# Kernel optimization log

Measured on AMD Instinct MI355X. Metric: run time of the kernel, lower is better.

## Reference

```python
import jax, jax.numpy as jnp
import numpy as np

N = 8192
C_IN = 512
C_INTER = 128  # in_channels // unit_nums = 512 // 4


def setup_inputs() -> dict:
    key = jax.random.key(0)
    ks = jax.random.split(key, 6)
    x = jax.random.normal(ks[0], (N, C_IN), dtype=jnp.float32)
    # Linear weights init: normal(0, 0.01); biases zero. Stored as [in, out].
    Wg = 0.01 * jax.random.normal(ks[1], (C_IN, C_INTER), dtype=jnp.float32)
    Wt = 0.01 * jax.random.normal(ks[2], (C_IN, C_INTER), dtype=jnp.float32)
    Wp = 0.01 * jax.random.normal(ks[3], (C_IN, C_INTER), dtype=jnp.float32)
    bg = jnp.zeros((C_INTER,), dtype=jnp.float32)
    bt = jnp.zeros((C_INTER,), dtype=jnp.float32)
    bp = jnp.zeros((C_INTER,), dtype=jnp.float32)
    # 1x1 conv weight (1, 2*C_INTER, 1, 1) flattened: first half hits theta, second half phi
    wcat = 0.01 * jax.random.normal(ks[4], (2 * C_INTER,), dtype=jnp.float32)
    return {"x": x, "Wg": Wg, "bg": bg, "Wt": Wt, "bt": bt, "Wp": Wp, "bp": bp, "wcat": wcat}


def reference(x, Wg, bg, Wt, bt, Wp, bp, wcat):
    n = x.shape[0]
    g_x = x @ Wg + bg          # [N, C_inter]
    theta = x @ Wt + bt        # [N, C_inter]
    phi = x @ Wp + bp          # [N, C_inter]
    c = theta.shape[1]
    # 1x1 conv over cat([theta_i, phi_j]) == w1.theta_i + w2.phi_j (outer sum), then ReLU
    a = theta @ wcat[:c]       # [N]
    b = phi @ wcat[c:]         # [N]
    f = jax.nn.relu(a[:, None] + b[None, :])  # [N, N]
    z = (f / n) @ g_x          # [N, C_inter]
    return z
```

## Files before the change

### kernel.cpp

```cpp
#include <hip/hip_runtime.h>

#define C_IN   512
#define C_INT  128
#define NBUCK  8192
#define SEG    32
#define NSEG   256

typedef short short8 __attribute__((ext_vector_type(8)));
typedef float floatx4 __attribute__((ext_vector_type(4)));


__device__ __forceinline__ int bucket_of(float v, float bmin, float inv_w) {
    float fk = (v - bmin) * inv_w;
    fk = fminf(fmaxf(fk, 0.f), (float)(NBUCK - 1));
    return (int)fk;
}

__device__ __forceinline__ short bf16rnd(float v) {
    unsigned u = __float_as_uint(v);
    return (short)((u + 0x7fffu + ((u >> 16) & 1u)) >> 16);
}


__global__ __launch_bounds__(256) void prep_kernel(
        const float* __restrict__ Wt, const float* __restrict__ Wp,
        const float* __restrict__ Wg, const float* __restrict__ wcat,
        const float* __restrict__ bt, const float* __restrict__ bp,
        float* __restrict__ ut, float* __restrict__ up, float* __restrict__ scal,
        unsigned short* __restrict__ WgT) {
    int t = threadIdx.x, bk = blockIdx.x;
    if (bk < 16) {
        const float* W  = (bk < 8) ? Wt : Wp;
        const float* wv = wcat + ((bk < 8) ? 0 : C_INT);
        float* dst      = (bk < 8) ? ut : up;
        int k = (bk & 7) * 64 + (t >> 2);
        int q = t & 3;
        const float4* row = (const float4*)(W + (size_t)k * C_INT);
        const float4* cv4 = (const float4*)wv;
        float s = 0.f;
        #pragma unroll
        for (int i = 0; i < 8; ++i) {
            float4 a = row[q * 8 + i];
            float4 c = cv4[q * 8 + i];
            s += a.x * c.x + a.y * c.y + a.z * c.z + a.w * c.w;
        }
        s += __shfl_xor(s, 1);
        s += __shfl_xor(s, 2);
        if (q == 0) dst[k] = s;
    } else if (bk == 16) {
        float sumsq = 0.f;
        const float4* w2v = (const float4*)(wcat + C_INT);
        for (int r = 0; r < 2; ++r) {
            int k = t * 2 + r;
            const float4* row = (const float4*)(Wp + (size_t)k * C_INT);
            float d = 0.f;
            #pragma unroll
            for (int i = 0; i < 32; ++i) {
                float4 a4 = row[i]; float4 c4 = w2v[i];
                d += a4.x * c4.x + a4.y * c4.y + a4.z * c4.z + a4.w * c4.w;
            }
            sumsq += d * d;
        }
        float s1p = (t < C_INT) ? bt[t] * wcat[t] : 0.f;
        float s2p = (t < C_INT) ? bp[t] * wcat[C_INT + t] : 0.f;
        for (int off = 32; off; off >>= 1) {
            s1p   += __shfl_down(s1p, off);
            s2p   += __shfl_down(s2p, off);
            sumsq += __shfl_down(sumsq, off);
        }
        __shared__ float red[12];
        int w = t >> 6, lane = t & 63;
        if (lane == 0) { red[w] = s1p; red[4 + w] = s2p; red[8 + w] = sumsq; }
        __syncthreads();
        if (t == 0) {
            float s0 = red[0] + red[1] + red[2] + red[3];
            float s1 = red[4] + red[5] + red[6] + red[7];
            float sq = red[8] + red[9] + red[10] + red[11];
            float sigma = sqrtf(sq);
            scal[0] = s0; scal[1] = s1;
            if (sigma > 1e-20f) {
                scal[2] = s1 - 8.f * sigma;
                scal[3] = (float)NBUCK / (16.f * sigma);
            } else {
                scal[2] = s1 - 1.f; scal[3] = 0.f;
            }
        }
    } else {
        __shared__ float tile[64][132];
        int kb = (bk - 17) * 64;
        #pragma unroll
        for (int it = 0; it < 8; ++it) {
            int idx = it * 256 + t;
            int r = idx >> 5, c4 = idx & 31;
            *(float4*)&tile[r][c4 * 4] =
                ((const float4*)(Wg + (size_t)(kb + r) * C_INT))[c4];
        }
        __syncthreads();
        int n = t & 127, kc = (t >> 7) * 32;
        unsigned pk[16];
        #pragma unroll
        for (int i = 0; i < 16; ++i) {
            unsigned lo = (unsigned short)bf16rnd(tile[kc + 2 * i][n]);
            unsigned hi = (unsigned short)bf16rnd(tile[kc + 2 * i + 1][n]);
            pk[i] = lo | (hi << 16);
        }
        uint4* dst = (uint4*)(WgT + (size_t)n * C_IN + kb + kc);
        #pragma unroll
        for (int i2 = 0; i2 < 4; ++i2) dst[i2] = *(uint4*)&pk[i2 * 4];
    }
}


__global__ __launch_bounds__(64) void gemm_mfma(
        const float* __restrict__ x, const unsigned short* __restrict__ WgT,
        const float* __restrict__ bg,
        const float* __restrict__ ut, const float* __restrict__ up,
        const float* __restrict__ scal,
        _Float16* __restrict__ g, float* __restrict__ a, float* __restrict__ b) {
    int lane = threadIdx.x;
    int i0 = blockIdx.x * 16;
    int m = lane & 15, q = lane >> 4;
    floatx4 accg[8] = {};
    floatx4 accab = {};
    const float* xrow = x + (size_t)(i0 + m) * C_IN + q * 8;
    const float* absrc = (m == 0) ? ut : up;
    #pragma unroll
    for (int ks = 0; ks < 16; ++ks) {
        int k0 = ks * 32;
        float4 f0 = *(const float4*)(xrow + k0);
        float4 f1 = *(const float4*)(xrow + k0 + 4);
        short8 af;
        af[0] = bf16rnd(f0.x); af[1] = bf16rnd(f0.y);
        af[2] = bf16rnd(f0.z); af[3] = bf16rnd(f0.w);
        af[4] = bf16rnd(f1.x); af[5] = bf16rnd(f1.y);
        af[6] = bf16rnd(f1.z); af[7] = bf16rnd(f1.w);
        short8 abf = {};
        if (m < 2) {
            float4 u0 = *(const float4*)(absrc + k0 + q * 8);
            float4 u1 = *(const float4*)(absrc + k0 + q * 8 + 4);
            abf[0] = bf16rnd(u0.x); abf[1] = bf16rnd(u0.y);
            abf[2] = bf16rnd(u0.z); abf[3] = bf16rnd(u0.w);
            abf[4] = bf16rnd(u1.x); abf[5] = bf16rnd(u1.y);
            abf[6] = bf16rnd(u1.z); abf[7] = bf16rnd(u1.w);
        }
        accab = __builtin_amdgcn_mfma_f32_16x16x32_bf16(af, abf, accab, 0, 0, 0);
        #pragma unroll
        for (int f = 0; f < 8; ++f) {
            short8 bfr = *(const short8*)(WgT + (size_t)(f * 16 + m) * C_IN + k0 + q * 8);
            accg[f] = __builtin_amdgcn_mfma_f32_16x16x32_bf16(af, bfr, accg[f], 0, 0, 0);
        }
    }
    #pragma unroll
    for (int f = 0; f < 8; ++f) {
        int col = f * 16 + m;
        float bgv = bg[col];
        #pragma unroll
        for (int r = 0; r < 4; ++r) {
            int row = i0 + q * 4 + r;
            g[(size_t)row * C_INT + col] = (_Float16)(accg[f][r] + bgv);
        }
    }
    if (m < 2) {
        float off = m ? scal[1] : scal[0];
        float* dst = m ? b : a;
        #pragma unroll
        for (int r = 0; r < 4; ++r) dst[i0 + q * 4 + r] = accab[r] + off;
    }
}


__global__ __launch_bounds__(1024) void sort_kernel(
        const float* __restrict__ b, const float* __restrict__ scal,
        unsigned* __restrict__ offs_g, unsigned short* __restrict__ perm_g,
        float* __restrict__ bsort_g) {
    __shared__ unsigned oh[NBUCK / 2];
    __shared__ unsigned cur[NBUCK / 2];
    __shared__ unsigned short ls[8192];
    __shared__ unsigned wtu[16];
    int t = threadIdx.x, lane = t & 63, wv = t >> 6;
    #pragma unroll
    for (int r = 0; r < 4; ++r) { oh[t + r * 1024] = 0u; cur[t + r * 1024] = 0u; }
    __syncthreads();
    float bmin = scal[2], inv_w = scal[3];
    int kb[8];
    float bv[8];
    #pragma unroll
    for (int r = 0; r < 8; ++r) {
        int j = t + r * 1024;
        bv[r] = b[j];
        kb[r] = bucket_of(bv[r], bmin, inv_w);
        atomicAdd(&oh[kb[r] >> 1], (kb[r] & 1) ? 0x10000u : 1u);
    }
    __syncthreads();
    unsigned h[8], p = 0;
    #pragma unroll
    for (int w = 0; w < 4; ++w) {
        unsigned word = oh[t * 4 + w];
        p += word & 0xffffu;  h[w * 2]     = p;
        p += word >> 16;      h[w * 2 + 1] = p;
    }
    unsigned v = p;
    #pragma unroll
    for (int d = 1; d < 64; d <<= 1) {
        unsigned u = __shfl_up(v, d);
        if (lane >= d) v += u;
    }
    if (lane == 63) wtu[wv] = v;
    __syncthreads();
    if (t < 16) {
        unsigned w = wtu[t];
        #pragma unroll
        for (int d = 1; d < 16; d <<= 1) {
            unsigned u = __shfl_up(w, d);
            if (t >= d) w += u;
        }
        wtu[t] = w;
    }
    __syncthreads();
    unsigned base = (v - p) + (wv ? wtu[wv - 1] : 0u);
    #pragma unroll
    for (int w = 0; w < 4; ++w) {
        unsigned lo = base + h[w * 2], hi = base + h[w * 2 + 1];
        oh[t * 4 + w] = lo | (hi << 16);
        offs_g[t * 8 + w * 2 + 1] = lo;
        offs_g[t * 8 + w * 2 + 2] = hi;
    }
    if (t == 0) offs_g[0] = 0u;
    __syncthreads();
    #pragma unroll
    for (int r = 0; r < 8; ++r) {
        int j = t + r * 1024;
        int k = kb[r];
        unsigned st = 0u;
        if (k > 0) {
            unsigned word = oh[(k - 1) >> 1];
            st = ((k - 1) & 1) ? (word >> 16) : (word & 0xffffu);
        }
        unsigned old = atomicAdd(&cur[k >> 1], (k & 1) ? 0x10000u : 1u);
        unsigned pos = (k & 1) ? (old >> 16) : (old & 0xffffu);
        ls[st + pos] = (unsigned short)j;
    }
    __syncthreads();
    #pragma unroll
    for (int r = 0; r < 8; ++r) {
        int e = t + r * 1024;
        int j = ls[e];
        perm_g[e] = (unsigned short)j;
        bsort_g[e] = b[j];
    }
}


__global__ __launch_bounds__(128) void segsum_kernel(
        const _Float16* __restrict__ g, const unsigned short* __restrict__ perm,
        const float* __restrict__ bsort,
        float* __restrict__ seg1, float* __restrict__ seg2) {
    __shared__ int pj[SEG];
    __shared__ float pb[SEG];
    int s = blockIdx.x, t = threadIdx.x;
    if (t < SEG) { pj[t] = perm[s * SEG + t]; pb[t] = bsort[s * SEG + t]; }
    __syncthreads();
    float a1 = 0.f, a2 = 0.f;
    #pragma unroll
    for (int e = 0; e < SEG; ++e) {
        float gv = (float)g[(size_t)pj[e] * C_INT + t];
        a1 += gv; a2 += pb[e] * gv;
    }
    seg1[s * C_INT + t] = a1;
    seg2[s * C_INT + t] = a2;
}


__global__ __launch_bounds__(128) void expand_kernel(
        const _Float16* __restrict__ g, const unsigned short* __restrict__ perm,
        const float* __restrict__ bsort,
        const float* __restrict__ seg1, const float* __restrict__ seg2,
        float* __restrict__ Pr1, float* __restrict__ Pr2) {
    __shared__ int pj[SEG];
    __shared__ float pb[SEG];
    int s = blockIdx.x, t = threadIdx.x;
    if (t < SEG) { pj[t] = perm[s * SEG + t]; pb[t] = bsort[s * SEG + t]; }
    __syncthreads();
    float r1 = 0.f, r2 = 0.f;
    for (int s2 = s + 1; s2 < NSEG; ++s2) {
        r1 += seg1[s2 * C_INT + t];
        r2 += seg2[s2 * C_INT + t];
    }
    #pragma unroll
    for (int e = SEG - 1; e >= 0; --e) {
        float gv = (float)g[(size_t)pj[e] * C_INT + t];
        r1 += gv; r2 += pb[e] * gv;
        size_t idx = (size_t)(s * SEG + e) * C_INT + t;
        Pr1[idx] = r1; Pr2[idx] = r2;
    }
    if (s == NSEG - 1) {
        Pr1[(size_t)8192 * C_INT + t] = 0.f;
        Pr2[(size_t)8192 * C_INT + t] = 0.f;
    }
}


__global__ __launch_bounds__(128) void out_kernel(
        const float* __restrict__ a, const float* __restrict__ scal,
        const _Float16* __restrict__ g,
        const unsigned* __restrict__ offs, const unsigned short* __restrict__ perm,
        const float* __restrict__ bsort,
        const float* __restrict__ Pr1, const float* __restrict__ Pr2,
        float* __restrict__ out, float inv_n) {
    __shared__ int pj[128];
    __shared__ float pb[128];
    int i = blockIdx.x, c = threadIdx.x;
    float ai = a[i], thr = -ai;
    float bmin = scal[2], inv_w = scal[3];
    int ki = bucket_of(thr, bmin, inv_w);
    unsigned e0 = offs[ki], e1 = offs[ki + 1];
    size_t base = (size_t)e1 * C_INT + c;
    float acc = ai * Pr1[base] + Pr2[base];
    for (unsigned be = e0; be < e1; be += 128) {
        unsigned cnt = min(128u, e1 - be);
        if ((unsigned)c < cnt) { pj[c] = perm[be + c]; pb[c] = bsort[be + c]; }
        __syncthreads();
        for (unsigned r = 0; r < cnt; ++r) {
            float bj = pb[r];
            if (bj > thr)
                acc += (ai + bj) * (float)g[(size_t)pj[r] * C_INT + c];
        }
        __syncthreads();
    }
    out[(size_t)i * C_INT + c] = acc * inv_n;
}


extern "C" void kernel_launch(void* const* d_in, const int* in_sizes, int n_in,
                              void* d_out, int out_size, void* d_ws, size_t ws_size,
                              hipStream_t stream) {
    const float* x    = (const float*)d_in[0];
    const float* Wg   = (const float*)d_in[1];
    const float* bg   = (const float*)d_in[2];
    const float* Wt   = (const float*)d_in[3];
    const float* bt   = (const float*)d_in[4];
    const float* Wp   = (const float*)d_in[5];
    const float* bp   = (const float*)d_in[6];
    const float* wcat = (const float*)d_in[7];
    float* out = (float*)d_out;
    int n = in_sizes[0] / C_IN;

    char* w = (char*)d_ws;
    size_t off = 0;
    auto alloc = [&](size_t bytes) -> void* {
        void* p = w + off;
        off += (bytes + 255) & ~(size_t)255;
        return p;
    };
    float*          ut    = (float*)alloc(C_IN * 4);
    float*          up    = (float*)alloc(C_IN * 4);
    float*          scal  = (float*)alloc(16);
    float*          a     = (float*)alloc((size_t)n * 4);
    float*          b     = (float*)alloc((size_t)n * 4);
    unsigned*       offs  = (unsigned*)alloc((size_t)(NBUCK + 1) * 4);
    unsigned short* perm  = (unsigned short*)alloc((size_t)n * 2);
    float*          bsort = (float*)alloc((size_t)n * 4);
    _Float16*       g     = (_Float16*)alloc((size_t)n * C_INT * 2);
    unsigned short* WgT   = (unsigned short*)alloc((size_t)C_INT * C_IN * 2);
    float*          seg1  = (float*)alloc((size_t)NSEG * C_INT * 4);
    float*          seg2  = (float*)alloc((size_t)NSEG * C_INT * 4);
    float*          Pr1   = (float*)alloc((size_t)(n + 1) * C_INT * 4);
    float*          Pr2   = (float*)alloc((size_t)(n + 1) * C_INT * 4);

    prep_kernel<<<25, 256, 0, stream>>>(Wt, Wp, Wg, wcat, bt, bp, ut, up, scal, WgT);
    gemm_mfma<<<n / 16, 64, 0, stream>>>(x, WgT, bg, ut, up, scal, g, a, b);
    sort_kernel<<<1, 1024, 0, stream>>>(b, scal, offs, perm, bsort);
    segsum_kernel<<<NSEG, 128, 0, stream>>>(g, perm, bsort, seg1, seg2);
    expand_kernel<<<NSEG, 128, 0, stream>>>(g, perm, bsort, seg1, seg2, Pr1, Pr2);
    out_kernel<<<n, 128, 0, stream>>>(a, scal, g, offs, perm, bsort, Pr1, Pr2,
                                      out, 1.0f / (float)n);
}
```

Before: 160.4 us.

## Split GEMM K dimension across four waves with LDS reduction

The projection GEMM kernel now launches 256 threads per 16-row block, with each of four waves handling a quarter of the K range. Partial accumulators from waves 1-3 are written to shared memory, and wave 0 adds them and writes the outputs. This shortens the serial MFMA chain per block and adds latency hiding via more waves. The cost is an LDS round trip, a block barrier, and higher LDS use that may limit occupancy.

```diff
diff --git a/kernel.cpp b/kernel.cpp
--- a/kernel.cpp
+++ b/kernel.cpp
@@ -111,13 +111,17 @@
 }
 
 
-__global__ __launch_bounds__(64) void gemm_mfma(
+#define RSTR 66
+
+__global__ __launch_bounds__(256) void gemm_mfma(
         const float* __restrict__ x, const unsigned short* __restrict__ WgT,
         const float* __restrict__ bg,
         const float* __restrict__ ut, const float* __restrict__ up,
         const float* __restrict__ scal,
         _Float16* __restrict__ g, float* __restrict__ a, float* __restrict__ b) {
-    int lane = threadIdx.x;
+    __shared__ float red[3][36][RSTR];
+    int tid = threadIdx.x;
+    int lane = tid & 63, wv = tid >> 6;
     int i0 = blockIdx.x * 16;
     int m = lane & 15, q = lane >> 4;
     floatx4 accg[8] = {};
@@ -125,8 +129,8 @@
     const float* xrow = x + (size_t)(i0 + m) * C_IN + q * 8;
     const float* absrc = (m == 0) ? ut : up;
     #pragma unroll
-    for (int ks = 0; ks < 16; ++ks) {
-        int k0 = ks * 32;
+    for (int ks = 0; ks < 4; ++ks) {
+        int k0 = (wv * 4 + ks) * 32;
         float4 f0 = *(const float4*)(xrow + k0);
         float4 f1 = *(const float4*)(xrow + k0 + 4);
         short8 af;
@@ -150,21 +154,45 @@
             accg[f] = __builtin_amdgcn_mfma_f32_16x16x32_bf16(af, bfr, accg[f], 0, 0, 0);
         }
     }
-    #pragma unroll
-    for (int f = 0; f < 8; ++f) {
-        int col = f * 16 + m;
-        float bgv = bg[col];
-        #pragma unroll
-        for (int r = 0; r < 4; ++r) {
-            int row = i0 + q * 4 + r;
-            g[(size_t)row * C_INT + col] = (_Float16)(accg[f][r] + bgv);
-        }
-    }
-    if (m < 2) {
-        float off = m ? scal[1] : scal[0];
-        float* dst = m ? b : a;
-        #pragma unroll
-        for (int r = 0; r < 4; ++r) dst[i0 + q * 4 + r] = accab[r] + off;
+    if (wv) {
+        #pragma unroll
+        for (int f = 0; f < 8; ++f)
+            #pragma unroll
+            for (int r = 0; r < 4; ++r)
+                red[wv - 1][f * 4 + r][lane] = accg[f][r];
+        #pragma unroll
+        for (int r = 0; r < 4; ++r)
+            red[wv - 1][32 + r][lane] = accab[r];
+    }
+    __syncthreads();
+    if (wv == 0) {
+        #pragma unroll
+        for (int w = 0; w < 3; ++w) {
+            #pragma unroll
+            for (int f = 0; f < 8; ++f)
+                #pragma unroll
+                for (int r = 0; r < 4; ++r)
+                    accg[f][r] += red[w][f * 4 + r][lane];
+            #pragma unroll
+            for (int r = 0; r < 4; ++r)
+                accab[r] += red[w][32 + r][lane];
+        }
+        #pragma unroll
+        for (int f = 0; f < 8; ++f) {
+            int col = f * 16 + m;
+            float bgv = bg[col];
+            #pragma unroll
+            for (int r = 0; r < 4; ++r) {
+                int row = i0 + q * 4 + r;
+                g[(size_t)row * C_INT + col] = (_Float16)(accg[f][r] + bgv);
+            }
+        }
+        if (m < 2) {
+            float off = m ? scal[1] : scal[0];
+            float* dst = m ? b : a;
+            #pragma unroll
+            for (int r = 0; r < 4; ++r) dst[i0 + q * 4 + r] = accab[r] + off;
+        }
     }
 }
 
@@ -183,12 +211,10 @@
     __syncthreads();
     float bmin = scal[2], inv_w = scal[3];
     int kb[8];
-    float bv[8];
     #pragma unroll
     for (int r = 0; r < 8; ++r) {
         int j = t + r * 1024;
-        bv[r] = b[j];
-        kb[r] = bucket_of(bv[r], bmin, inv_w);
+        kb[r] = bucket_of(b[j], bmin, inv_w);
         atomicAdd(&oh[kb[r] >> 1], (kb[r] & 1) ? 0x10000u : 1u);
     }
     __syncthreads();
@@ -368,7 +394,7 @@
     float*          Pr2   = (float*)alloc((size_t)(n + 1) * C_INT * 4);
 
     prep_kernel<<<25, 256, 0, stream>>>(Wt, Wp, Wg, wcat, bt, bp, ut, up, scal, WgT);
-    gemm_mfma<<<n / 16, 64, 0, stream>>>(x, WgT, bg, ut, up, scal, g, a, b);
+    gemm_mfma<<<n / 16, 256, 0, stream>>>(x, WgT, bg, ut, up, scal, g, a, b);
     sort_kernel<<<1, 1024, 0, stream>>>(b, scal, offs, perm, bsort);
     segsum_kernel<<<NSEG, 128, 0, stream>>>(g, perm, bsort, seg1, seg2);
     expand_kernel<<<NSEG, 128, 0, stream>>>(g, perm, bsort, seg1, seg2, Pr1, Pr2);
```

After: 151.8 us. -5.3%, faster.
